# Kernel optimization log

Hardware: AMD Instinct MI355X
Metric: run time of the kernel (lower is better)

The kernel has to match this reference:

```python
import jax, jax.numpy as jnp
import numpy as np

N_NODES = 100000
N_EDGES = 3200000
OUT_DIM = 128


def setup_inputs() -> dict:
    key = jax.random.key(0)
    k1, k2, k3, k4, k5, k6 = jax.random.split(key, 6)
    return {
        "previous_inclusion_score": jax.random.normal(k1, (N_NODES,), dtype=jnp.float32),
        "nodes": jax.random.normal(k2, (N_NODES, 3), dtype=jnp.float32),
        "row_indices": jax.random.randint(k3, (N_EDGES,), 0, N_NODES, dtype=jnp.int32),
        "col_indices": jax.random.randint(k4, (N_EDGES,), 0, N_NODES, dtype=jnp.int32),
        "W_phi": jax.random.normal(k5, (OUT_DIM,), dtype=jnp.float32),
        "W_theta": jax.random.normal(k6, (3, 1), dtype=jnp.float32),
    }


def reference(previous_inclusion_score, nodes, row_indices, col_indices, W_phi, W_theta):
    # gather endpoints and project 3D differences through W_theta: [E,3] @ [3,1] -> [E,1]
    diff = nodes[row_indices] - nodes[col_indices]
    proj = diff @ W_theta
    # torch.norm over dim=1 of an [E,1] tensor == abs
    neigh_distances = jnp.abs(proj[:, 0])  # [E]
    # per-node max over incident edges; empty segments -> -inf, original leaves them 0
    max_distances = jax.ops.segment_max(neigh_distances, row_indices, num_segments=N_NODES)
    max_distances = jnp.maximum(max_distances, 0.0)  # distances are >= 0, so this matches the zeros default
    # outer product with W_phi: [N, D]
    list_inc_score = W_phi[None, :] * max_distances[:, None]
    # previous_inclusion_score is non-empty and D != 1 -> mean over feature dim, then average with previous
    inc_mean = jnp.mean(list_inc_score, axis=1)  # [N]
    return 0.5 * (previous_inclusion_score + inc_mean)
```

## Files before the change

### kernel.cpp

```cpp
#include <hip/hip_runtime.h>

#define OUT_DIM 128
#define CHUNK_LG 15
#define CHUNK (1 << CHUNK_LG)
#define PB 64

typedef int          vint4  __attribute__((ext_vector_type(4)));
typedef unsigned int vuint4 __attribute__((ext_vector_type(4)));
typedef unsigned int u32;

__device__ __forceinline__ u32 enc15(float d) {
    u32 b = __float_as_uint(d);
    b += 0x7FFFu + ((b >> 16) & 1u);
    return (b >> 16) & 0x7FFFu;
}

__global__ void init_kernel(float* __restrict__ p, float* __restrict__ meanW,
                            const float* __restrict__ nodes,
                            const float* __restrict__ Wt,
                            const float* __restrict__ W_phi, int n) {
    int i = blockIdx.x * blockDim.x + threadIdx.x;
    if (i < n) {
        float x = nodes[3 * i], y = nodes[3 * i + 1], z = nodes[3 * i + 2];
        p[i] = x * Wt[0] + y * Wt[1] + z * Wt[2];
    }
    if (blockIdx.x == 0 && threadIdx.x == 0) {
        float s = 0.0f;
        #pragma unroll
        for (int j = 0; j < OUT_DIM; ++j) s += W_phi[j];
        *meanW = s / (float)OUT_DIM;
    }
}

__global__ void encode_kernel(const float* __restrict__ p,
                              const int* __restrict__ row,
                              const int* __restrict__ col,
                              u32* __restrict__ key, int E) {
    int t = blockIdx.x * blockDim.x + threadIdx.x;
    int base = t * 4;
    if (base >= E) return;
    if (base + 3 < E) {
        vint4 r = __builtin_nontemporal_load((const vint4*)(row + base));
        vint4 c = __builtin_nontemporal_load((const vint4*)(col + base));
        float d0 = fabsf(p[r.x] - p[c.x]);
        float d1 = fabsf(p[r.y] - p[c.y]);
        float d2 = fabsf(p[r.z] - p[c.z]);
        float d3 = fabsf(p[r.w] - p[c.w]);
        vuint4 k;
        k.x = ((u32)r.x << 15) | enc15(d0);
        k.y = ((u32)r.y << 15) | enc15(d1);
        k.z = ((u32)r.z << 15) | enc15(d2);
        k.w = ((u32)r.w << 15) | enc15(d3);
        *(vuint4*)(key + base) = k;
    } else {
        for (int e = base; e < E; ++e)
            key[e] = ((u32)row[e] << 15) | enc15(fabsf(p[row[e]] - p[col[e]]));
    }
}

#define PROC(V) do { \
        if ((V.x >> (15 + CHUNK_LG)) == uc) atomicMax(&lds[(V.x >> 15) & (CHUNK - 1)], V.x & 0x7FFFu); \
        if ((V.y >> (15 + CHUNK_LG)) == uc) atomicMax(&lds[(V.y >> 15) & (CHUNK - 1)], V.y & 0x7FFFu); \
        if ((V.z >> (15 + CHUNK_LG)) == uc) atomicMax(&lds[(V.z >> 15) & (CHUNK - 1)], V.z & 0x7FFFu); \
        if ((V.w >> (15 + CHUNK_LG)) == uc) atomicMax(&lds[(V.w >> 15) & (CHUNK - 1)], V.w & 0x7FFFu); \
    } while (0)

__global__ __launch_bounds__(512) void chunkmax_kernel(const u32* __restrict__ key,
                                                       u32* __restrict__ partial,
                                                       int E, int nch) {
    __shared__ u32 lds[CHUNK];
    int c = blockIdx.x / PB;
    int b = blockIdx.x % PB;
    vuint4 zero = {0u, 0u, 0u, 0u};
    vuint4* lds4 = (vuint4*)lds;
    for (int i = threadIdx.x; i < CHUNK / 4; i += 512) lds4[i] = zero;
    __syncthreads();

    int G = E >> 2;
    int per = (G + PB - 1) / PB;
    int s = b * per;
    int e = min(s + per, G);
    const vuint4* key4 = (const vuint4*)key;
    u32 uc = (u32)c;
    const int step = 512;
    int k = s + (int)threadIdx.x;
    for (; k + 3 * step < e; k += 4 * step) {
        vuint4 a0 = key4[k];
        vuint4 a1 = key4[k + step];
        vuint4 a2 = key4[k + 2 * step];
        vuint4 a3 = key4[k + 3 * step];
        PROC(a0); PROC(a1); PROC(a2); PROC(a3);
    }
    for (; k < e; k += step) {
        vuint4 a0 = key4[k];
        PROC(a0);
    }
    if (b == PB - 1) {
        for (int j = (G << 2) + (int)threadIdx.x; j < E; j += step) {
            u32 v = key[j];
            if ((v >> (15 + CHUNK_LG)) == uc) atomicMax(&lds[(v >> 15) & (CHUNK - 1)], v & 0x7FFFu);
        }
    }
    __syncthreads();
    u32* dst = partial + ((size_t)c * PB + b) * (CHUNK / 2);
    for (int j = threadIdx.x; j < CHUNK / 2; j += 512)
        dst[j] = lds[2 * j] | (lds[2 * j + 1] << 16);
}

__global__ void reduce_final_kernel(const float* __restrict__ prev,
                                    const u32* __restrict__ partial,
                                    const float* __restrict__ meanW,
                                    float* __restrict__ out, int n) {
    int t = blockIdx.x * blockDim.x + threadIdx.x;
    int i0 = t * 2;
    if (i0 >= n) return;
    int chunk = i0 >> CHUNK_LG;
    int local = i0 & (CHUNK - 1);
    const u32* base = partial + (size_t)chunk * PB * (CHUNK / 2) + (local >> 1);
    u32 mlo = 0, mhi = 0;
    #pragma unroll
    for (int b = 0; b < PB; ++b) {
        u32 v = base[(size_t)b * (CHUNK / 2)];
        mlo = max(mlo, v & 0xFFFFu);
        mhi = max(mhi, v >> 16);
    }
    float mw = *meanW;
    float flo = __uint_as_float(mlo << 16);
    float fhi = __uint_as_float(mhi << 16);
    out[i0] = 0.5f * (prev[i0] + mw * flo);
    if (i0 + 1 < n)
        out[i0 + 1] = 0.5f * (prev[i0 + 1] + mw * fhi);
}

__global__ void fb_zero_kernel(float* __restrict__ maxd, float* __restrict__ p,
                               float* __restrict__ meanW,
                               const float* __restrict__ nodes,
                               const float* __restrict__ Wt,
                               const float* __restrict__ W_phi, int n) {
    int i = blockIdx.x * blockDim.x + threadIdx.x;
    if (i < n) {
        maxd[i] = 0.0f;
        float x = nodes[3 * i], y = nodes[3 * i + 1], z = nodes[3 * i + 2];
        p[i] = x * Wt[0] + y * Wt[1] + z * Wt[2];
    }
    if (blockIdx.x == 0 && threadIdx.x == 0) {
        float s = 0.0f;
        for (int j = 0; j < OUT_DIM; ++j) s += W_phi[j];
        *meanW = s / (float)OUT_DIM;
    }
}
__global__ void fb_edge_kernel(const float* __restrict__ p,
                               const int* __restrict__ row,
                               const int* __restrict__ col,
                               float* __restrict__ maxd, int E) {
    int t = blockIdx.x * blockDim.x + threadIdx.x;
    int base = t * 4;
    if (base >= E) return;
    if (base + 3 < E) {
        vint4 r = __builtin_nontemporal_load((const vint4*)(row + base));
        vint4 c = __builtin_nontemporal_load((const vint4*)(col + base));
        atomicMax((int*)&maxd[r.x], __float_as_int(fabsf(p[r.x] - p[c.x])));
        atomicMax((int*)&maxd[r.y], __float_as_int(fabsf(p[r.y] - p[c.y])));
        atomicMax((int*)&maxd[r.z], __float_as_int(fabsf(p[r.z] - p[c.z])));
        atomicMax((int*)&maxd[r.w], __float_as_int(fabsf(p[r.w] - p[c.w])));
    } else {
        for (int e = base; e < E; ++e) {
            float d = fabsf(p[row[e]] - p[col[e]]);
            atomicMax((int*)&maxd[row[e]], __float_as_int(d));
        }
    }
}
__global__ void fb_final_kernel(const float* __restrict__ prev,
                                const float* __restrict__ maxd,
                                const float* __restrict__ meanW,
                                float* __restrict__ out, int n) {
    int i = blockIdx.x * blockDim.x + threadIdx.x;
    if (i < n) out[i] = 0.5f * (prev[i] + (*meanW) * maxd[i]);
}

extern "C" void kernel_launch(void* const* d_in, const int* in_sizes, int n_in,
                              void* d_out, int out_size, void* d_ws, size_t ws_size,
                              hipStream_t stream) {
    const float* prev    = (const float*)d_in[0];
    const float* nodes   = (const float*)d_in[1];
    const int*   row     = (const int*)d_in[2];
    const int*   col     = (const int*)d_in[3];
    const float* W_phi   = (const float*)d_in[4];
    const float* W_theta = (const float*)d_in[5];

    const int N = in_sizes[0];
    const int E = in_sizes[2];
    float* out = (float*)d_out;
    const int B = 256;

    const int nch = (N + CHUNK - 1) >> CHUNK_LG;

    size_t pBytes    = ((size_t)N * 4 + 15) & ~(size_t)15;
    size_t keyBytes  = (((size_t)E + 3) & ~(size_t)3) * 4;
    size_t partBytes = (size_t)nch * PB * (CHUNK / 2) * 4;
    size_t need = pBytes + keyBytes + partBytes + 4;

    if (ws_size >= need && N <= (1 << 17)) {
        float* p     = (float*)d_ws;
        u32*   key   = (u32*)((char*)d_ws + pBytes);
        u32*   part  = (u32*)((char*)d_ws + pBytes + keyBytes);
        float* meanW = (float*)((char*)d_ws + pBytes + keyBytes + partBytes);

        init_kernel<<<(N + B - 1) / B, B, 0, stream>>>(p, meanW, nodes, W_theta, W_phi, N);
        int tE = (E + 3) / 4;
        encode_kernel<<<(tE + B - 1) / B, B, 0, stream>>>(p, row, col, key, E);
        chunkmax_kernel<<<nch * PB, 512, 0, stream>>>(key, part, E, nch);
        int tN = (N + 1) / 2;
        reduce_final_kernel<<<(tN + B - 1) / B, B, 0, stream>>>(prev, part, meanW, out, N);
    } else {
        float* p     = (float*)d_ws;
        float* maxd  = (float*)d_ws + N;
        float* meanW = (float*)d_ws + 2 * (size_t)N;
        fb_zero_kernel<<<(N + B - 1) / B, B, 0, stream>>>(maxd, p, meanW, nodes, W_theta, W_phi, N);
        int tE = (E + 3) / 4;
        fb_edge_kernel<<<(tE + B - 1) / B, B, 0, stream>>>(p, row, col, maxd, E);
        fb_final_kernel<<<(N + B - 1) / B, B, 0, stream>>>(prev, maxd, meanW, out, N);
    }
}
```

Before: 56.95 us.

## Use non-power-of-two node chunks to cut key-scan passes in chunkmax

Replaces the 32768-node power-of-two chunk with a 36864-node chunk, so N=100000 needs 3 chunks instead of 4 and the key array is streamed three times instead of four. Chunk membership is now tested by subtract-and-compare against a chunk base. It also moves to 1024-thread blocks and 86 partial blocks per chunk, for 258 blocks in total, and partially unrolls the final reduction. The cost is a larger LDS footprint (144KB per block), integer division in the reduce step, and more partial buffers for the final reduction to combine.

New measurement: 71.58 us. 1.26x slower.

```diff
diff --git a/kernel.cpp b/kernel.cpp
--- a/kernel.cpp
+++ b/kernel.cpp
@@ -1,9 +1,9 @@
 #include <hip/hip_runtime.h>
 
 #define OUT_DIM 128
-#define CHUNK_LG 15
-#define CHUNK (1 << CHUNK_LG)
-#define PB 64
+#define CHUNKN 36864
+#define PB 86
+#define NCH_MAX 3
 
 typedef int          vint4  __attribute__((ext_vector_type(4)));
 typedef unsigned int vuint4 __attribute__((ext_vector_type(4)));
@@ -59,21 +59,21 @@
 }
 
 #define PROC(V) do { \
-        if ((V.x >> (15 + CHUNK_LG)) == uc) atomicMax(&lds[(V.x >> 15) & (CHUNK - 1)], V.x & 0x7FFFu); \
-        if ((V.y >> (15 + CHUNK_LG)) == uc) atomicMax(&lds[(V.y >> 15) & (CHUNK - 1)], V.y & 0x7FFFu); \
-        if ((V.z >> (15 + CHUNK_LG)) == uc) atomicMax(&lds[(V.z >> 15) & (CHUNK - 1)], V.z & 0x7FFFu); \
-        if ((V.w >> (15 + CHUNK_LG)) == uc) atomicMax(&lds[(V.w >> 15) & (CHUNK - 1)], V.w & 0x7FFFu); \
+        u32 rx = (V.x >> 15) - cbase; if (rx < CHUNKN) atomicMax(&lds[rx], V.x & 0x7FFFu); \
+        u32 ry = (V.y >> 15) - cbase; if (ry < CHUNKN) atomicMax(&lds[ry], V.y & 0x7FFFu); \
+        u32 rz = (V.z >> 15) - cbase; if (rz < CHUNKN) atomicMax(&lds[rz], V.z & 0x7FFFu); \
+        u32 rw = (V.w >> 15) - cbase; if (rw < CHUNKN) atomicMax(&lds[rw], V.w & 0x7FFFu); \
     } while (0)
 
-__global__ __launch_bounds__(512) void chunkmax_kernel(const u32* __restrict__ key,
-                                                       u32* __restrict__ partial,
-                                                       int E, int nch) {
-    __shared__ u32 lds[CHUNK];
+__global__ __launch_bounds__(1024) void chunkmax_kernel(const u32* __restrict__ key,
+                                                        u32* __restrict__ partial,
+                                                        int E, int nch) {
+    __shared__ u32 lds[CHUNKN];
     int c = blockIdx.x / PB;
     int b = blockIdx.x % PB;
     vuint4 zero = {0u, 0u, 0u, 0u};
     vuint4* lds4 = (vuint4*)lds;
-    for (int i = threadIdx.x; i < CHUNK / 4; i += 512) lds4[i] = zero;
+    for (int i = threadIdx.x; i < CHUNKN / 4; i += 1024) lds4[i] = zero;
     __syncthreads();
 
     int G = E >> 2;
@@ -81,8 +81,8 @@
     int s = b * per;
     int e = min(s + per, G);
     const vuint4* key4 = (const vuint4*)key;
-    u32 uc = (u32)c;
-    const int step = 512;
+    u32 cbase = (u32)c * CHUNKN;
+    const int step = 1024;
     int k = s + (int)threadIdx.x;
     for (; k + 3 * step < e; k += 4 * step) {
         vuint4 a0 = key4[k];
@@ -98,12 +98,13 @@
     if (b == PB - 1) {
         for (int j = (G << 2) + (int)threadIdx.x; j < E; j += step) {
             u32 v = key[j];
-            if ((v >> (15 + CHUNK_LG)) == uc) atomicMax(&lds[(v >> 15) & (CHUNK - 1)], v & 0x7FFFu);
+            u32 rel = (v >> 15) - cbase;
+            if (rel < CHUNKN) atomicMax(&lds[rel], v & 0x7FFFu);
         }
     }
     __syncthreads();
-    u32* dst = partial + ((size_t)c * PB + b) * (CHUNK / 2);
-    for (int j = threadIdx.x; j < CHUNK / 2; j += 512)
+    u32* dst = partial + ((size_t)c * PB + b) * (CHUNKN / 2);
+    for (int j = threadIdx.x; j < CHUNKN / 2; j += 1024)
         dst[j] = lds[2 * j] | (lds[2 * j + 1] << 16);
 }
 
@@ -114,13 +115,13 @@
     int t = blockIdx.x * blockDim.x + threadIdx.x;
     int i0 = t * 2;
     if (i0 >= n) return;
-    int chunk = i0 >> CHUNK_LG;
-    int local = i0 & (CHUNK - 1);
-    const u32* base = partial + (size_t)chunk * PB * (CHUNK / 2) + (local >> 1);
+    int chunk = i0 / CHUNKN;
+    int local = i0 - chunk * CHUNKN;
+    const u32* base = partial + (size_t)chunk * PB * (CHUNKN / 2) + (local >> 1);
     u32 mlo = 0, mhi = 0;
-    #pragma unroll
+    #pragma unroll 2
     for (int b = 0; b < PB; ++b) {
-        u32 v = base[(size_t)b * (CHUNK / 2)];
+        u32 v = base[(size_t)b * (CHUNKN / 2)];
         mlo = max(mlo, v & 0xFFFFu);
         mhi = max(mhi, v >> 16);
     }
@@ -193,14 +194,14 @@
     float* out = (float*)d_out;
     const int B = 256;
 
-    const int nch = (N + CHUNK - 1) >> CHUNK_LG;
+    const int nch = (N + CHUNKN - 1) / CHUNKN;
 
     size_t pBytes    = ((size_t)N * 4 + 15) & ~(size_t)15;
     size_t keyBytes  = (((size_t)E + 3) & ~(size_t)3) * 4;
-    size_t partBytes = (size_t)nch * PB * (CHUNK / 2) * 4;
+    size_t partBytes = (size_t)nch * PB * (CHUNKN / 2) * 4;
     size_t need = pBytes + keyBytes + partBytes + 4;
 
-    if (ws_size >= need && N <= (1 << 17)) {
+    if (ws_size >= need && N <= NCH_MAX * CHUNKN && N <= (1 << 17)) {
         float* p     = (float*)d_ws;
         u32*   key   = (u32*)((char*)d_ws + pBytes);
         u32*   part  = (u32*)((char*)d_ws + pBytes + keyBytes);
@@ -209,7 +210,7 @@
         init_kernel<<<(N + B - 1) / B, B, 0, stream>>>(p, meanW, nodes, W_theta, W_phi, N);
         int tE = (E + 3) / 4;
         encode_kernel<<<(tE + B - 1) / B, B, 0, stream>>>(p, row, col, key, E);
-        chunkmax_kernel<<<nch * PB, 512, 0, stream>>>(key, part, E, nch);
+        chunkmax_kernel<<<nch * PB, 1024, 0, stream>>>(key, part, E, nch);
         int tN = (N + 1) / 2;
         reduce_final_kernel<<<(tN + B - 1) / B, B, 0, stream>>>(prev, part, meanW, out, N);
     } else {
```
